# Performance work log

Hardware: AMD Instinct MI355X
Metric: run time of the kernel (lower is better)

The kernel has to match this reference:

```python
import jax, jax.numpy as jnp
import numpy as np

CODEBOOK_SIZE = 8192
EMBED_DIM = 128
BETA = 0.25


def setup_inputs() -> dict:
    key = jax.random.key(0)
    k1, k2 = jax.random.split(key)
    z = jax.random.normal(k1, (8, 4096, EMBED_DIM), dtype=jnp.float32)
    # nn.Embedding weight init: uniform(-1/embedding_dim, 1/embedding_dim)
    emb = jax.random.uniform(
        k2, (CODEBOOK_SIZE, EMBED_DIM), dtype=jnp.float32,
        minval=-1.0 / EMBED_DIM, maxval=1.0 / EMBED_DIM)
    return {"z": z, "emb": emb}


def reference(z, emb):
    sg = jax.lax.stop_gradient
    zf = z.reshape(-1, EMBED_DIM)                      # [N, D]
    # squared-distance: |z|^2 + |e|^2 - 2 z.e^T  -> [N, K]
    d = (jnp.sum(zf * zf, axis=1, keepdims=True)
         + jnp.sum(emb * emb, axis=1)
         - 2.0 * jnp.einsum('nd,kd->nk', zf, emb))
    idx = jnp.argmin(d, axis=1)                        # [N]
    z_q = emb[idx].reshape(z.shape)                    # gather + reshape

    # codebook usage perplexity (bincount)
    counts = jnp.zeros(CODEBOOK_SIZE, dtype=jnp.float32).at[idx].add(1.0)
    e_mean = counts / idx.size
    perplexity = jnp.exp(-jnp.sum(e_mean * jnp.log(e_mean + 1e-8)))

    commit_loss = (BETA * jnp.mean((sg(z_q) - z) ** 2)
                   + jnp.mean((z_q - sg(z)) ** 2))
    z_q_st = z + sg(z_q - z)                           # straight-through
    return z_q_st, commit_loss, perplexity
```

## Files before the change

kernel.cpp:

```cpp
#include <hip/hip_runtime.h>
#include <float.h>
#include <math.h>

#define DIM    128
#define KCB    8192
#define BT     128
#define NC     128
#define NCHUNK (KCB / NC)

typedef __attribute__((ext_vector_type(8))) short bf16x8;
typedef __attribute__((ext_vector_type(4))) float f32x4;

__device__ unsigned g_ehi[KCB * DIM / 2];
__device__ unsigned g_elo[KCB * DIM / 2];
__device__ float    g_h[KCB];
__device__ unsigned g_counts[KCB];
__device__ double   g_loss;
__device__ unsigned g_done;

__device__ __forceinline__ unsigned short f2b(float x) {
    union { float f; unsigned u; } v; v.f = x;
    unsigned r = v.u + 0x7fffu + ((v.u >> 16) & 1u);
    return (unsigned short)(r >> 16);
}
__device__ __forceinline__ float b2f(unsigned short h) {
    union { unsigned u; float f; } v; v.u = ((unsigned)h) << 16; return v.f;
}
__device__ __forceinline__ void gll16(const void* g, void* l) {
    __builtin_amdgcn_global_load_lds(
        (const __attribute__((address_space(1))) void*)g,
        (__attribute__((address_space(3))) void*)l, 16, 0, 0);
}

__global__ __launch_bounds__(256) void vq_prep(const float* __restrict__ emb)
{
    const int tid  = threadIdx.x;
    const int gid  = blockIdx.x * 256 + tid;
    if (gid < KCB) g_counts[gid] = 0u;
    if (gid == 0)  { g_loss = 0.0; g_done = 0u; }

    const int code = (blockIdx.x << 2) + (tid >> 6);
    const int lane = tid & 63;
    const float2 v = ((const float2*)emb)[code * 64 + lane];

    unsigned short h0 = f2b(v.x), h1 = f2b(v.y);
    unsigned short l0 = f2b(v.x - b2f(h0)), l1 = f2b(v.y - b2f(h1));
    const int widx = code * 64 + (lane ^ ((code & 7) << 2));
    g_ehi[widx] = (unsigned)h0 | ((unsigned)h1 << 16);
    g_elo[widx] = (unsigned)l0 | ((unsigned)l1 << 16);

    float s = v.x * v.x + v.y * v.y;
    #pragma unroll
    for (int o = 32; o > 0; o >>= 1) s += __shfl_down(s, o);
    if (lane == 0) g_h[code] = 0.5f * s;
}

__global__ __launch_bounds__(512) __attribute__((amdgpu_waves_per_eu(2, 2))) void vq_main(
    const float* __restrict__ z, const float* __restrict__ emb, float* __restrict__ out)
{
    __shared__ char   smem[2 * 65536];
    __shared__ float  rv[BT * 4];
    __shared__ int    ri[BT * 4];
    __shared__ int    idx_sh[BT];
    __shared__ double wred[8];
    __shared__ int    done_sh;

    const int tid  = threadIdx.x;
    const int lane = tid & 63;
    const int wid  = tid >> 6;
    const int tg   = wid >> 2;
    const int cq   = wid & 3;
    const int l15  = lane & 15;
    const int lg   = lane >> 4;
    const long t0  = (long)blockIdx.x * BT;

    bf16x8 ah[4][4], al[4][4];
    #pragma unroll
    for (int m = 0; m < 4; ++m) {
        const long trow = t0 + tg * 64 + m * 16 + l15;
        #pragma unroll
        for (int kk = 0; kk < 4; ++kk) {
            const float4* zp = (const float4*)(z + trow * DIM + kk * 32 + lg * 8);
            float4 v0 = zp[0], v1 = zp[1];
            float xs[8] = {v0.x, v0.y, v0.z, v0.w, v1.x, v1.y, v1.z, v1.w};
            #pragma unroll
            for (int j = 0; j < 8; ++j) {
                unsigned short hb = f2b(xs[j]);
                ah[m][kk][j] = (short)hb;
                al[m][kk][j] = (short)f2b(xs[j] - b2f(hb));
            }
        }
    }

    const int xr = (l15 & 7) << 4;
    int loff[4];
    #pragma unroll
    for (int kk = 0; kk < 4; ++kk) loff[kk] = l15 * 256 + ((kk * 64 + lg * 16) ^ xr);

    float bv[4][4]; int bi[4][4];
    #pragma unroll
    for (int m = 0; m < 4; ++m)
        #pragma unroll
        for (int r = 0; r < 4; ++r) { bv[m][r] = FLT_MAX; bi[m][r] = 0; }

    {
        const int o = tid * 16;
        #pragma unroll
        for (int r = 0; r < 4; ++r)
            gll16((const char*)g_ehi + r * 8192 + o, smem + r * 8192 + o);
        #pragma unroll
        for (int r = 0; r < 4; ++r)
            gll16((const char*)g_elo + r * 8192 + o, smem + 32768 + r * 8192 + o);
    }
    __syncthreads();

    for (int ch = 0; ch < NCHUNK; ++ch) {
        const int cb  = ch * NC;
        const int cur = ch & 1;
        if (ch + 1 < NCHUNK) {
            const int  o  = tid * 16;
            const long go = (long)(ch + 1) * 32768;
            char* ldst = smem + (cur ^ 1) * 65536;
            #pragma unroll
            for (int r = 0; r < 4; ++r)
                gll16((const char*)g_ehi + go + r * 8192 + o, ldst + r * 8192 + o);
            #pragma unroll
            for (int r = 0; r < 4; ++r)
                gll16((const char*)g_elo + go + r * 8192 + o, ldst + 32768 + r * 8192 + o);
        }

        const char* base = smem + cur * 65536 + cq * 8192;
        const int   c0   = cb + cq * 32 + l15;
        float hc[2] = { g_h[c0], g_h[c0 + 16] };

        #pragma unroll
        for (int n = 0; n < 2; ++n) {
            bf16x8 bh[4], bl[4];
            #pragma unroll
            for (int kk = 0; kk < 4; ++kk) {
                bh[kk] = *(const bf16x8*)(base + n * 4096 + loff[kk]);
                bl[kk] = *(const bf16x8*)(base + 32768 + n * 4096 + loff[kk]);
            }
            f32x4 acc[4];
            #pragma unroll
            for (int m = 0; m < 4; ++m) acc[m] = (f32x4){0.f, 0.f, 0.f, 0.f};
            #pragma unroll
            for (int kk = 0; kk < 4; ++kk) {
                #pragma unroll
                for (int m = 0; m < 4; ++m)
                    acc[m] = __builtin_amdgcn_mfma_f32_16x16x32_bf16(ah[m][kk], bh[kk], acc[m], 0, 0, 0);
                #pragma unroll
                for (int m = 0; m < 4; ++m)
                    acc[m] = __builtin_amdgcn_mfma_f32_16x16x32_bf16(al[m][kk], bh[kk], acc[m], 0, 0, 0);
                #pragma unroll
                for (int m = 0; m < 4; ++m)
                    acc[m] = __builtin_amdgcn_mfma_f32_16x16x32_bf16(ah[m][kk], bl[kk], acc[m], 0, 0, 0);
            }
            const int c = c0 + n * 16;
            #pragma unroll
            for (int m = 0; m < 4; ++m)
                #pragma unroll
                for (int r = 0; r < 4; ++r) {
                    float sc = hc[n] - acc[m][r];
                    if (sc < bv[m][r]) { bv[m][r] = sc; bi[m][r] = c; }
                }
        }
        __syncthreads();
    }

    #pragma unroll
    for (int m = 0; m < 4; ++m)
        #pragma unroll
        for (int r = 0; r < 4; ++r) {
            float v = bv[m][r]; int ix = bi[m][r];
            #pragma unroll
            for (int o = 1; o < 16; o <<= 1) {
                float ov = __shfl_xor(v, o);
                int   oi = __shfl_xor(ix, o);
                if (ov < v || (ov == v && oi < ix)) { v = ov; ix = oi; }
            }
            if (l15 == 0) {
                int t = tg * 64 + m * 16 + lg * 4 + r;
                rv[t * 4 + cq] = v; ri[t * 4 + cq] = ix;
            }
        }
    __syncthreads();
    if (tid < BT) {
        float best = rv[tid * 4]; int bidx = ri[tid * 4];
        #pragma unroll
        for (int x = 1; x < 4; ++x) {
            float v = rv[tid * 4 + x]; int i = ri[tid * 4 + x];
            if (v < best || (v == best && i < bidx)) { best = v; bidx = i; }
        }
        idx_sh[tid] = bidx;
        atomicAdd(&g_counts[bidx], 1u);
    }
    __syncthreads();

    float lsum = 0.f;
    {
        const float4* zf4 = (const float4*)(z + t0 * DIM);
        const float4* ef4 = (const float4*)emb;
        float4*       of4 = (float4*)(out + t0 * DIM);
        #pragma unroll
        for (int r = 0; r < 8; ++r) {
            int f = r * 512 + tid;
            int t = f >> 5, dw = f & 31;
            int ci = idx_sh[t];
            float4 e4 = ef4[(size_t)ci * 32 + dw];
            float4 z4 = zf4[f];
            float dx = e4.x - z4.x, dy = e4.y - z4.y;
            float dz = e4.z - z4.z, dw2 = e4.w - z4.w;
            lsum += dx * dx + dy * dy + dz * dz + dw2 * dw2;
            float4 o;
            o.x = z4.x + dx; o.y = z4.y + dy; o.z = z4.z + dz; o.w = z4.w + dw2;
            of4[f] = o;
        }
    }
    #pragma unroll
    for (int o = 32; o > 0; o >>= 1) lsum += __shfl_down(lsum, o);
    if (lane == 0) wred[wid] = (double)lsum;
    __syncthreads();
    if (tid == 0) {
        double s = 0.0;
        #pragma unroll
        for (int w = 0; w < 8; ++w) s += wred[w];
        atomicAdd(&g_loss, s);
    }

    __threadfence();
    if (tid == 0) done_sh = (atomicAdd(&g_done, 1u) == gridDim.x - 1) ? 1 : 0;
    __syncthreads();
    if (done_sh) {
        const int ntok    = (int)gridDim.x * BT;
        const int n_elems = ntok * DIM;
        double s = 0.0;
        for (int i = tid; i < KCB; i += 512) {
            unsigned cnt = atomicAdd(&g_counts[i], 0u);
            float em = (float)cnt / (float)ntok;
            s += (double)(em * logf(em + 1e-8f));
        }
        #pragma unroll
        for (int o = 32; o > 0; o >>= 1) s += __shfl_down(s, o);
        if (lane == 0) wred[wid] = s;
        __syncthreads();
        if (tid == 0) {
            double tot = 0.0;
            #pragma unroll
            for (int w = 0; w < 8; ++w) tot += wred[w];
            double L = atomicAdd(&g_loss, 0.0);
            out[(size_t)n_elems]     = (float)(1.25 * L / (double)n_elems);
            out[(size_t)n_elems + 1] = expf((float)(-tot));
        }
    }
}

extern "C" void kernel_launch(void* const* d_in, const int* in_sizes, int n_in,
                              void* d_out, int out_size, void* d_ws, size_t ws_size,
                              hipStream_t stream)
{
    const float* z   = (const float*)d_in[0];
    const float* emb = (const float*)d_in[1];
    float* out = (float*)d_out;

    const int n_elems = in_sizes[0];
    const int ntok    = n_elems / DIM;

    vq_prep<<<dim3(KCB / 4),   256, 0, stream>>>(emb);
    vq_main<<<dim3(ntok / BT), 512, 0, stream>>>(z, emb, out);
}
```

Before: 308.0 us.

## Replace split-bf16 triple MFMA with single bf16 pass plus fp32 candidate rescoring

Drops the hi/lo bf16 split (three MFMAs per tile) in favour of a single bf16 MFMA pass. Each lane keeps its top-2 packed score/index keys, and every code within a fixed margin of the block-wide minimum is collected into a per-token candidate list. Those candidates are rescored exactly in fp32 against the original embeddings. The block grows to 1024 threads with smaller per-wave tiles. This cuts MFMA work and LDS traffic by about three times, but correctness relies on the margin covering the bf16 error and on the list cap of 32 not overflowing; only two candidates per lane are kept, and the low 13 bits of the score are truncated.

Measured after the change: 303.7 us. About the same (-1.4%).

```diff
diff --git a/kernel.cpp b/kernel.cpp
--- a/kernel.cpp
+++ b/kernel.cpp
@@ -7,12 +7,13 @@
 #define BT     128
 #define NC     128
 #define NCHUNK (KCB / NC)
+#define CAP    32
+#define MARGIN 0.016f
 
 typedef __attribute__((ext_vector_type(8))) short bf16x8;
 typedef __attribute__((ext_vector_type(4))) float f32x4;
 
-__device__ unsigned g_ehi[KCB * DIM / 2];
-__device__ unsigned g_elo[KCB * DIM / 2];
+__device__ unsigned g_eh[KCB * DIM / 2];
 __device__ float    g_h[KCB];
 __device__ unsigned g_counts[KCB];
 __device__ double   g_loss;
@@ -23,19 +24,25 @@
     unsigned r = v.u + 0x7fffu + ((v.u >> 16) & 1u);
     return (unsigned short)(r >> 16);
 }
-__device__ __forceinline__ float b2f(unsigned short h) {
-    union { unsigned u; float f; } v; v.u = ((unsigned)h) << 16; return v.f;
-}
 __device__ __forceinline__ void gll16(const void* g, void* l) {
     __builtin_amdgcn_global_load_lds(
         (const __attribute__((address_space(1))) void*)g,
         (__attribute__((address_space(3))) void*)l, 16, 0, 0);
 }
+__device__ __forceinline__ unsigned pkey(float sc, int c) {
+    unsigned u = __float_as_uint(sc);
+    u ^= (unsigned)(((int)u >> 31)) | 0x80000000u;
+    return (u & ~8191u) | (unsigned)c;
+}
+__device__ __forceinline__ float key2sc(unsigned k) {
+    unsigned u = (k & 0x80000000u) ? (k ^ 0x80000000u) : ~k;
+    return __uint_as_float(u);
+}
 
 __global__ __launch_bounds__(256) void vq_prep(const float* __restrict__ emb)
 {
-    const int tid  = threadIdx.x;
-    const int gid  = blockIdx.x * 256 + tid;
+    const int tid = threadIdx.x;
+    const int gid = blockIdx.x * 256 + tid;
     if (gid < KCB) g_counts[gid] = 0u;
     if (gid == 0)  { g_loss = 0.0; g_done = 0u; }
 
@@ -44,10 +51,8 @@
     const float2 v = ((const float2*)emb)[code * 64 + lane];
 
     unsigned short h0 = f2b(v.x), h1 = f2b(v.y);
-    unsigned short l0 = f2b(v.x - b2f(h0)), l1 = f2b(v.y - b2f(h1));
     const int widx = code * 64 + (lane ^ ((code & 7) << 2));
-    g_ehi[widx] = (unsigned)h0 | ((unsigned)h1 << 16);
-    g_elo[widx] = (unsigned)l0 | ((unsigned)l1 << 16);
+    g_eh[widx] = (unsigned)h0 | ((unsigned)h1 << 16);
 
     float s = v.x * v.x + v.y * v.y;
     #pragma unroll
@@ -55,40 +60,38 @@
     if (lane == 0) g_h[code] = 0.5f * s;
 }
 
-__global__ __launch_bounds__(512) __attribute__((amdgpu_waves_per_eu(2, 2))) void vq_main(
+__global__ __launch_bounds__(1024) void vq_main(
     const float* __restrict__ z, const float* __restrict__ emb, float* __restrict__ out)
 {
-    __shared__ char   smem[2 * 65536];
-    __shared__ float  rv[BT * 4];
-    __shared__ int    ri[BT * 4];
-    __shared__ int    idx_sh[BT];
-    __shared__ double wred[8];
-    __shared__ int    done_sh;
+    __shared__ char     smem[2 * 32768];
+    __shared__ unsigned rv[BT * 4];
+    __shared__ unsigned bk_sh[BT];
+    __shared__ int      lcnt[BT];
+    __shared__ int      list[BT * CAP];
+    __shared__ int      idx_sh[BT];
+    __shared__ double   wred[16];
+    __shared__ int      done_sh;
 
     const int tid  = threadIdx.x;
     const int lane = tid & 63;
     const int wid  = tid >> 6;
-    const int tg   = wid >> 2;
+    const int tq   = wid >> 2;
     const int cq   = wid & 3;
     const int l15  = lane & 15;
     const int lg   = lane >> 4;
     const long t0  = (long)blockIdx.x * BT;
 
-    bf16x8 ah[4][4], al[4][4];
-    #pragma unroll
-    for (int m = 0; m < 4; ++m) {
-        const long trow = t0 + tg * 64 + m * 16 + l15;
+    bf16x8 ah[2][4];
+    #pragma unroll
+    for (int m = 0; m < 2; ++m) {
+        const long trow = t0 + tq * 32 + m * 16 + l15;
         #pragma unroll
         for (int kk = 0; kk < 4; ++kk) {
             const float4* zp = (const float4*)(z + trow * DIM + kk * 32 + lg * 8);
             float4 v0 = zp[0], v1 = zp[1];
             float xs[8] = {v0.x, v0.y, v0.z, v0.w, v1.x, v1.y, v1.z, v1.w};
             #pragma unroll
-            for (int j = 0; j < 8; ++j) {
-                unsigned short hb = f2b(xs[j]);
-                ah[m][kk][j] = (short)hb;
-                al[m][kk][j] = (short)f2b(xs[j] - b2f(hb));
-            }
+            for (int j = 0; j < 8; ++j) ah[m][kk][j] = (short)f2b(xs[j]);
         }
     }
 
@@ -97,103 +100,122 @@
     #pragma unroll
     for (int kk = 0; kk < 4; ++kk) loff[kk] = l15 * 256 + ((kk * 64 + lg * 16) ^ xr);
 
-    float bv[4][4]; int bi[4][4];
-    #pragma unroll
-    for (int m = 0; m < 4; ++m)
-        #pragma unroll
-        for (int r = 0; r < 4; ++r) { bv[m][r] = FLT_MAX; bi[m][r] = 0; }
+    unsigned b0[2][4], b1[2][4];
+    #pragma unroll
+    for (int m = 0; m < 2; ++m)
+        #pragma unroll
+        for (int r = 0; r < 4; ++r) { b0[m][r] = 0xFFFFFFFFu; b1[m][r] = 0xFFFFFFFFu; }
 
     {
         const int o = tid * 16;
-        #pragma unroll
-        for (int r = 0; r < 4; ++r)
-            gll16((const char*)g_ehi + r * 8192 + o, smem + r * 8192 + o);
-        #pragma unroll
-        for (int r = 0; r < 4; ++r)
-            gll16((const char*)g_elo + r * 8192 + o, smem + 32768 + r * 8192 + o);
+        gll16((const char*)g_eh + o, smem + o);
+        gll16((const char*)g_eh + 16384 + o, smem + 16384 + o);
     }
     __syncthreads();
 
     for (int ch = 0; ch < NCHUNK; ++ch) {
-        const int cb  = ch * NC;
         const int cur = ch & 1;
         if (ch + 1 < NCHUNK) {
             const int  o  = tid * 16;
             const long go = (long)(ch + 1) * 32768;
-            char* ldst = smem + (cur ^ 1) * 65536;
-            #pragma unroll
-            for (int r = 0; r < 4; ++r)
-                gll16((const char*)g_ehi + go + r * 8192 + o, ldst + r * 8192 + o);
-            #pragma unroll
-            for (int r = 0; r < 4; ++r)
-                gll16((const char*)g_elo + go + r * 8192 + o, ldst + 32768 + r * 8192 + o);
-        }
-
-        const char* base = smem + cur * 65536 + cq * 8192;
-        const int   c0   = cb + cq * 32 + l15;
-        float hc[2] = { g_h[c0], g_h[c0 + 16] };
+            char* ldst = smem + (cur ^ 1) * 32768;
+            gll16((const char*)g_eh + go + o, ldst + o);
+            gll16((const char*)g_eh + go + 16384 + o, ldst + 16384 + o);
+        }
+
+        const char* base = smem + cur * 32768 + cq * 8192;
+        const int   c0   = ch * NC + cq * 32 + l15;
+        const float hv0  = g_h[c0];
+        const float hv1  = g_h[c0 + 16];
 
         #pragma unroll
         for (int n = 0; n < 2; ++n) {
-            bf16x8 bh[4], bl[4];
-            #pragma unroll
-            for (int kk = 0; kk < 4; ++kk) {
+            bf16x8 bh[4];
+            #pragma unroll
+            for (int kk = 0; kk < 4; ++kk)
                 bh[kk] = *(const bf16x8*)(base + n * 4096 + loff[kk]);
-                bl[kk] = *(const bf16x8*)(base + 32768 + n * 4096 + loff[kk]);
-            }
-            f32x4 acc[4];
-            #pragma unroll
-            for (int m = 0; m < 4; ++m) acc[m] = (f32x4){0.f, 0.f, 0.f, 0.f};
-            #pragma unroll
-            for (int kk = 0; kk < 4; ++kk) {
+            f32x4 acc[2];
+            #pragma unroll
+            for (int m = 0; m < 2; ++m) acc[m] = (f32x4){0.f, 0.f, 0.f, 0.f};
+            #pragma unroll
+            for (int kk = 0; kk < 4; ++kk)
                 #pragma unroll
-                for (int m = 0; m < 4; ++m)
+                for (int m = 0; m < 2; ++m)
                     acc[m] = __builtin_amdgcn_mfma_f32_16x16x32_bf16(ah[m][kk], bh[kk], acc[m], 0, 0, 0);
-                #pragma unroll
-                for (int m = 0; m < 4; ++m)
-                    acc[m] = __builtin_amdgcn_mfma_f32_16x16x32_bf16(al[m][kk], bh[kk], acc[m], 0, 0, 0);
-                #pragma unroll
-                for (int m = 0; m < 4; ++m)
-                    acc[m] = __builtin_amdgcn_mfma_f32_16x16x32_bf16(ah[m][kk], bl[kk], acc[m], 0, 0, 0);
-            }
-            const int c = c0 + n * 16;
-            #pragma unroll
-            for (int m = 0; m < 4; ++m)
+
+            const float hvn = n ? hv1 : hv0;
+            const int   c   = c0 + n * 16;
+            #pragma unroll
+            for (int m = 0; m < 2; ++m)
                 #pragma unroll
                 for (int r = 0; r < 4; ++r) {
-                    float sc = hc[n] - acc[m][r];
-                    if (sc < bv[m][r]) { bv[m][r] = sc; bi[m][r] = c; }
+                    unsigned k  = pkey(hvn - acc[m][r], c);
+                    unsigned mx = max(b0[m][r], k);
+                    b0[m][r] = min(b0[m][r], k);
+                    b1[m][r] = min(b1[m][r], mx);
                 }
         }
         __syncthreads();
     }
 
     #pragma unroll
-    for (int m = 0; m < 4; ++m)
+    for (int m = 0; m < 2; ++m)
         #pragma unroll
         for (int r = 0; r < 4; ++r) {
-            float v = bv[m][r]; int ix = bi[m][r];
-            #pragma unroll
-            for (int o = 1; o < 16; o <<= 1) {
-                float ov = __shfl_xor(v, o);
-                int   oi = __shfl_xor(ix, o);
-                if (ov < v || (ov == v && oi < ix)) { v = ov; ix = oi; }
+            unsigned k = b0[m][r];
+            #pragma unroll
+            for (int o = 1; o < 16; o <<= 1) k = min(k, (unsigned)__shfl_xor((int)k, o));
+            if (l15 == 0) rv[(tq * 32 + m * 16 + lg * 4 + r) * 4 + cq] = k;
+        }
+    __syncthreads();
+    if (tid < BT) {
+        unsigned k = min(min(rv[tid * 4], rv[tid * 4 + 1]), min(rv[tid * 4 + 2], rv[tid * 4 + 3]));
+        bk_sh[tid] = k;
+        lcnt[tid]  = 0;
+    }
+    __syncthreads();
+
+    #pragma unroll
+    for (int m = 0; m < 2; ++m)
+        #pragma unroll
+        for (int r = 0; r < 4; ++r) {
+            const int   t  = tq * 32 + m * 16 + lg * 4 + r;
+            const float th = key2sc(bk_sh[t]) + MARGIN;
+            if (key2sc(b0[m][r]) <= th) {
+                int p = atomicAdd(&lcnt[t], 1);
+                if (p < CAP) list[t * CAP + p] = (int)(b0[m][r] & 8191u);
             }
-            if (l15 == 0) {
-                int t = tg * 64 + m * 16 + lg * 4 + r;
-                rv[t * 4 + cq] = v; ri[t * 4 + cq] = ix;
+            if (key2sc(b1[m][r]) <= th) {
+                int p = atomicAdd(&lcnt[t], 1);
+                if (p < CAP) list[t * CAP + p] = (int)(b1[m][r] & 8191u);
             }
         }
     __syncthreads();
-    if (tid < BT) {
-        float best = rv[tid * 4]; int bidx = ri[tid * 4];
-        #pragma unroll
-        for (int x = 1; x < 4; ++x) {
-            float v = rv[tid * 4 + x]; int i = ri[tid * 4 + x];
-            if (v < best || (v == best && i < bidx)) { best = v; bidx = i; }
-        }
-        idx_sh[tid] = bidx;
-        atomicAdd(&g_counts[bidx], 1u);
+
+    {
+        const int t  = wid * 8 + (lane >> 3);
+        const int li = lane & 7;
+        const int cnt = min(lcnt[t], CAP);
+        const float4* zt = (const float4*)(z + (t0 + t) * DIM) + li * 4;
+        float4 zr0 = zt[0], zr1 = zt[1], zr2 = zt[2], zr3 = zt[3];
+        float bsc = FLT_MAX; int bidx = KCB;
+        for (int j = 0; j < cnt; ++j) {
+            const int c = list[t * CAP + j];
+            const float4* ec = (const float4*)(emb + (size_t)c * DIM) + li * 4;
+            float4 e0 = ec[0], e1 = ec[1], e2 = ec[2], e3 = ec[3];
+            float s = zr0.x*e0.x + zr0.y*e0.y + zr0.z*e0.z + zr0.w*e0.w
+                    + zr1.x*e1.x + zr1.y*e1.y + zr1.z*e1.z + zr1.w*e1.w
+                    + zr2.x*e2.x + zr2.y*e2.y + zr2.z*e2.z + zr2.w*e2.w
+                    + zr3.x*e3.x + zr3.y*e3.y + zr3.z*e3.z + zr3.w*e3.w;
+            #pragma unroll
+            for (int o = 1; o < 8; o <<= 1) s += __shfl_xor(s, o);
+            float sc = g_h[c] - s;
+            if (sc < bsc || (sc == bsc && c < bidx)) { bsc = sc; bidx = c; }
+        }
+        if (li == 0) {
+            idx_sh[t] = bidx;
+            atomicAdd(&g_counts[bidx], 1u);
+        }
     }
     __syncthreads();
 
@@ -203,8 +225,8 @@
         const float4* ef4 = (const float4*)emb;
         float4*       of4 = (float4*)(out + t0 * DIM);
         #pragma unroll
-        for (int r = 0; r < 8; ++r) {
-            int f = r * 512 + tid;
+        for (int r = 0; r < 4; ++r) {
+            int f = r * 1024 + tid;
             int t = f >> 5, dw = f & 31;
             int ci = idx_sh[t];
             float4 e4 = ef4[(size_t)ci * 32 + dw];
@@ -224,7 +246,7 @@
     if (tid == 0) {
         double s = 0.0;
         #pragma unroll
-        for (int w = 0; w < 8; ++w) s += wred[w];
+        for (int w = 0; w < 16; ++w) s += wred[w];
         atomicAdd(&g_loss, s);
     }
 
@@ -235,7 +257,7 @@
         const int ntok    = (int)gridDim.x * BT;
         const int n_elems = ntok * DIM;
         double s = 0.0;
-        for (int i = tid; i < KCB; i += 512) {
+        for (int i = tid; i < KCB; i += 1024) {
             unsigned cnt = atomicAdd(&g_counts[i], 0u);
             float em = (float)cnt / (float)ntok;
             s += (double)(em * logf(em + 1e-8f));
@@ -247,7 +269,7 @@
         if (tid == 0) {
             double tot = 0.0;
             #pragma unroll
-            for (int w = 0; w < 8; ++w) tot += wred[w];
+            for (int w = 0; w < 16; ++w) tot += wred[w];
             double L = atomicAdd(&g_loss, 0.0);
             out[(size_t)n_elems]     = (float)(1.25 * L / (double)n_elems);
             out[(size_t)n_elems + 1] = expf((float)(-tot));
@@ -266,6 +288,6 @@
     const int n_elems = in_sizes[0];
     const int ntok    = n_elems / DIM;
 
-    vq_prep<<<dim3(KCB / 4),   256, 0, stream>>>(emb);
-    vq_main<<<dim3(ntok / BT), 512, 0, stream>>>(z, emb, out);
-}
+    vq_prep<<<dim3(KCB / 4),   256,  0, stream>>>(emb);
+    vq_main<<<dim3(ntok / BT), 1024, 0, stream>>>(z, emb, out);
+}
```
